# Kernel tuning notes

Measured on AMD Instinct MI355X. Metric: run time of the kernel, lower is better.

The kernel has to match this reference:

```python
import jax, jax.numpy as jnp
import numpy as np

N_NODES = 50000
N_EDGES = 600000
F_IN = 128
HID = 128
N_CLASSES = 10


def _gcn_graph(edge_index, n_nodes):
    # PyG GCNConv: add self-loops, deg computed on target (col) with weight 1,
    # norm_e = deg^-1/2[src] * deg^-1/2[dst]
    src = jnp.concatenate([edge_index[0], jnp.arange(n_nodes, dtype=edge_index.dtype)])
    dst = jnp.concatenate([edge_index[1], jnp.arange(n_nodes, dtype=edge_index.dtype)])
    deg = jax.ops.segment_sum(jnp.ones_like(dst, dtype=jnp.float32), dst, num_segments=n_nodes)
    dinv = jnp.where(deg > 0, jax.lax.rsqrt(deg), 0.0)
    norm = dinv[src] * dinv[dst]  # [E+N]
    return src, dst, norm


def _gcn_layer(x, W, b, src, dst, norm, n_nodes):
    h = x @ W                      # [N, out] linear first (bias applied post-agg)
    m = h[src] * norm[:, None]     # gather + scale, [E+N, out]
    out = jax.ops.segment_sum(m, dst, num_segments=n_nodes)  # scatter-add
    return out + b


def setup_inputs() -> dict:
    key = jax.random.key(0)
    ks = jax.random.split(key, 4)
    x = jax.random.normal(ks[0], (N_NODES, F_IN), dtype=jnp.float32)
    edge_index = jax.random.randint(ks[1], (2, N_EDGES), 0, N_NODES, dtype=jnp.int64)
    # Glorot-ish init scale for weights
    W_stack = jax.random.normal(ks[2], (8, HID, HID), dtype=jnp.float32) * (1.0 / np.sqrt(HID))
    b_stack = jnp.zeros((8, HID), dtype=jnp.float32)
    W_out = jax.random.normal(ks[3], (HID, N_CLASSES), dtype=jnp.float32) * (1.0 / np.sqrt(HID))
    b_out = jnp.zeros((N_CLASSES,), dtype=jnp.float32)
    return {"x": x, "edge_index": edge_index, "W_stack": W_stack, "b_stack": b_stack,
            "W_out": W_out, "b_out": b_out}


def reference(x, edge_index, W_stack, b_stack, W_out, b_out):
    n_nodes = x.shape[0]
    src, dst, norm = _gcn_graph(edge_index, n_nodes)
    h = x
    for i in range(8):  # conv1..conv8 with ELU
        h = jax.nn.elu(_gcn_layer(h, W_stack[i], b_stack[i], src, dst, norm, n_nodes))
    # conv9: no activation
    return _gcn_layer(h, W_out, b_out, src, dst, norm, n_nodes)
```

## Files before the change

### kernel.cpp

```cpp
#include <hip/hip_runtime.h>
#include <math.h>

#define NN 50000
#define NE 600000
#define HID 128
#define NCLS 10

typedef __bf16 bf16x8 __attribute__((ext_vector_type(8)));
typedef float f32x16 __attribute__((ext_vector_type(16)));

__device__ __forceinline__ void split3(float f, ushort& h, ushort& m, ushort& l) {
    unsigned uh = __float_as_uint(f) & 0xffff0000u;
    float fm = f - __uint_as_float(uh);
    unsigned um = __float_as_uint(fm) & 0xffff0000u;
    float fl = fm - __uint_as_float(um);
    h = (ushort)(uh >> 16);
    m = (ushort)(um >> 16);
    l = (ushort)(__float_as_uint(fl) >> 16);
}


__global__ __launch_bounds__(256) void k_count(const int* __restrict__ edge,
                                               int* __restrict__ counts) {
    int e = blockIdx.x * 256 + threadIdx.x;
    if (e < NE) atomicAdd(&counts[edge[NE + e]], 1);
}

__device__ __forceinline__ int wave_incl_scan(int x, int lane) {
#pragma unroll
    for (int off = 1; off < 64; off <<= 1) {
        int y = __shfl_up(x, off, 64);
        if (lane >= off) x += y;
    }
    return x;
}

__global__ __launch_bounds__(256) void k_scan1(const int* __restrict__ counts,
                                               int* __restrict__ rowptr,
                                               int* __restrict__ bsum,
                                               float* __restrict__ dinv) {
    __shared__ int ws[4];
    int tid = threadIdx.x;
    int i = blockIdx.x * 256 + tid;
    int lane = tid & 63, wv = tid >> 6;
    int v = (i < NN) ? counts[i] : 0;
    if (i < NN) dinv[i] = rsqrtf((float)(v + 1));
    int x = wave_incl_scan(v, lane);
    if (lane == 63) ws[wv] = x;
    __syncthreads();
    int off = 0;
    for (int j = 0; j < wv; ++j) off += ws[j];
    if (i < NN) rowptr[i] = off + x - v;
    if (tid == 255) bsum[blockIdx.x] = off + x;
}

__global__ __launch_bounds__(256) void k_scan2(int* __restrict__ bsum, int n) {
    __shared__ int ws[4];
    int tid = threadIdx.x;
    int lane = tid & 63, wv = tid >> 6;
    int v = (tid < n) ? bsum[tid] : 0;
    int x = wave_incl_scan(v, lane);
    if (lane == 63) ws[wv] = x;
    __syncthreads();
    int off = 0;
    for (int j = 0; j < wv; ++j) off += ws[j];
    __syncthreads();
    if (tid < n) bsum[tid] = off + x - v;
}

__global__ __launch_bounds__(256) void k_scan3(int* __restrict__ rowptr,
                                               const int* __restrict__ bsum) {
    int i = blockIdx.x * 256 + threadIdx.x;
    if (i < NN) rowptr[i] += bsum[blockIdx.x];
    if (i == 0) rowptr[NN] = NE;
}

__global__ __launch_bounds__(256) void k_fill(const int* __restrict__ edge,
                                              const int* __restrict__ rowptr,
                                              int* __restrict__ cursor,
                                              const float* __restrict__ dinv,
                                              int2* __restrict__ csr) {
    int e = blockIdx.x * 256 + threadIdx.x;
    if (e >= NE) return;
    int s = edge[e], d = edge[NE + e];
    int p = rowptr[d] + atomicAdd(&cursor[d], 1);
    csr[p] = make_int2(s, __float_as_int(dinv[s] * dinv[d]));
}


__global__ __launch_bounds__(256) void k_split_w(const float* __restrict__ Wst,
                                                 ushort* __restrict__ Wt3) {
    int i = blockIdx.x * 256 + threadIdx.x;
    if (i >= 8 * HID * HID) return;
    int l = i >> 14;
    int k = (i >> 7) & 127;
    int n = i & 127;
    ushort h, m, lo;
    split3(Wst[i], h, m, lo);
    size_t base = (size_t)l * 3 * HID * HID + (size_t)n * HID + k;
    Wt3[base] = h;
    Wt3[base + HID * HID] = m;
    Wt3[base + 2 * HID * HID] = lo;
}


__global__ __launch_bounds__(256) void k_mfma_gemm(const float* __restrict__ H,
                                                   const ushort* __restrict__ Wt,
                                                   float* __restrict__ T) {
    __shared__ ushort As[3][128][40];
    __shared__ ushort Bs[3][128][40];
    int tid = threadIdx.x;
    int lane = tid & 63, w = tid >> 6;
    int wy = w >> 1, wx = w & 1;
    int l31 = lane & 31, lh = lane >> 5;
    int rowbase = blockIdx.x * 128;

    int arow = tid >> 1;
    int kh = (tid & 1) * 16;
    int garow = rowbase + arow;
    if (garow >= NN) garow = NN - 1;
    size_t aoff = (size_t)garow * HID;

    f32x16 acc[2][2] = {};

    for (int k0 = 0; k0 < HID; k0 += 32) {
        const float4* asrc = (const float4*)(H + aoff + k0 + kh);
        float4 af0 = asrc[0], af1 = asrc[1], af2 = asrc[2], af3 = asrc[3];
        uint4 rb[6];
#pragma unroll
        for (int c = 0; c < 6; ++c) {
            int chunk = c * 256 + tid;
            int p = chunk >> 9;
            int rem = chunk & 511;
            int col = rem >> 2;
            int q = rem & 3;
            rb[c] = *(const uint4*)(Wt + p * (HID * HID) + col * HID + k0 + q * 8);
        }
        float av[16] = {af0.x, af0.y, af0.z, af0.w, af1.x, af1.y, af1.z, af1.w,
                        af2.x, af2.y, af2.z, af2.w, af3.x, af3.y, af3.z, af3.w};
        union { ushort u[16]; uint4 v[2]; } ph, pm, pl;
#pragma unroll
        for (int q = 0; q < 16; ++q) split3(av[q], ph.u[q], pm.u[q], pl.u[q]);

        __syncthreads();
        *(uint4*)&As[0][arow][kh] = ph.v[0];
        *(uint4*)&As[0][arow][kh + 8] = ph.v[1];
        *(uint4*)&As[1][arow][kh] = pm.v[0];
        *(uint4*)&As[1][arow][kh + 8] = pm.v[1];
        *(uint4*)&As[2][arow][kh] = pl.v[0];
        *(uint4*)&As[2][arow][kh + 8] = pl.v[1];
#pragma unroll
        for (int c = 0; c < 6; ++c) {
            int chunk = c * 256 + tid;
            int p = chunk >> 9;
            int rem = chunk & 511;
            int col = rem >> 2;
            int q = rem & 3;
            *(uint4*)&Bs[p][col][q * 8] = rb[c];
        }
        __syncthreads();

#pragma unroll
        for (int ks = 0; ks < 32; ks += 16) {
            int kk = ks + lh * 8;
            bf16x8 a[3][2], b[3][2];
#pragma unroll
            for (int p = 0; p < 3; ++p)
#pragma unroll
                for (int h = 0; h < 2; ++h) {
                    a[p][h] = *(const bf16x8*)&As[p][wy * 64 + h * 32 + l31][kk];
                    b[p][h] = *(const bf16x8*)&Bs[p][wx * 64 + h * 32 + l31][kk];
                }
#pragma unroll
            for (int h = 0; h < 2; ++h)
#pragma unroll
                for (int c = 0; c < 2; ++c)
                    acc[h][c] = __builtin_amdgcn_mfma_f32_32x32x16_bf16(a[0][h], b[0][c], acc[h][c], 0, 0, 0);
#pragma unroll
            for (int h = 0; h < 2; ++h)
#pragma unroll
                for (int c = 0; c < 2; ++c)
                    acc[h][c] = __builtin_amdgcn_mfma_f32_32x32x16_bf16(a[0][h], b[1][c], acc[h][c], 0, 0, 0);
#pragma unroll
            for (int h = 0; h < 2; ++h)
#pragma unroll
                for (int c = 0; c < 2; ++c)
                    acc[h][c] = __builtin_amdgcn_mfma_f32_32x32x16_bf16(a[1][h], b[0][c], acc[h][c], 0, 0, 0);
#pragma unroll
            for (int h = 0; h < 2; ++h)
#pragma unroll
                for (int c = 0; c < 2; ++c)
                    acc[h][c] = __builtin_amdgcn_mfma_f32_32x32x16_bf16(a[0][h], b[2][c], acc[h][c], 0, 0, 0);
#pragma unroll
            for (int h = 0; h < 2; ++h)
#pragma unroll
                for (int c = 0; c < 2; ++c)
                    acc[h][c] = __builtin_amdgcn_mfma_f32_32x32x16_bf16(a[1][h], b[1][c], acc[h][c], 0, 0, 0);
#pragma unroll
            for (int h = 0; h < 2; ++h)
#pragma unroll
                for (int c = 0; c < 2; ++c)
                    acc[h][c] = __builtin_amdgcn_mfma_f32_32x32x16_bf16(a[2][h], b[0][c], acc[h][c], 0, 0, 0);
        }
    }
#pragma unroll
    for (int h = 0; h < 2; ++h)
#pragma unroll
        for (int c = 0; c < 2; ++c)
#pragma unroll
            for (int reg = 0; reg < 16; ++reg) {
                int r = (reg & 3) + 8 * (reg >> 2) + 4 * lh;
                int gr = rowbase + wy * 64 + h * 32 + r;
                if (gr < NN)
                    T[(size_t)gr * HID + wx * 64 + c * 32 + l31] = acc[h][c][reg];
            }
}


__global__ __launch_bounds__(256) void k_gather_agg(const float* __restrict__ T,
                                                    float* __restrict__ Hout,
                                                    const int* __restrict__ rowptr,
                                                    const int2* __restrict__ csr,
                                                    const float* __restrict__ dinv,
                                                    const float* __restrict__ bias) {
    int node = (blockIdx.x * 256 + threadIdx.x) >> 5;
    if (node >= NN) return;
    int l31 = threadIdx.x & 31;

    int beg = rowptr[node], end = rowptr[node + 1];
    float sn = dinv[node];
    float4 bv = ((const float4*)bias)[l31];
    float4 tv = ((const float4*)(T + (size_t)node * HID))[l31];

    float4 acc = {0.f, 0.f, 0.f, 0.f};
    const int2 zed = make_int2(0, 0);

    int i = beg;
    int2 e0 = (i < end) ? csr[i] : zed;
    int2 e1 = (i + 1 < end) ? csr[i + 1] : zed;
    int2 e2 = (i + 2 < end) ? csr[i + 2] : zed;
    int2 e3 = (i + 3 < end) ? csr[i + 3] : zed;
    for (; i < end; i += 4) {
        float4 u0 = ((const float4*)(T + (size_t)e0.x * HID))[l31];
        float4 u1 = ((const float4*)(T + (size_t)e1.x * HID))[l31];
        float4 u2 = ((const float4*)(T + (size_t)e2.x * HID))[l31];
        float4 u3 = ((const float4*)(T + (size_t)e3.x * HID))[l31];
        float w0 = __int_as_float(e0.y), w1 = __int_as_float(e1.y);
        float w2 = __int_as_float(e2.y), w3 = __int_as_float(e3.y);
        e0 = (i + 4 < end) ? csr[i + 4] : zed;
        e1 = (i + 5 < end) ? csr[i + 5] : zed;
        e2 = (i + 6 < end) ? csr[i + 6] : zed;
        e3 = (i + 7 < end) ? csr[i + 7] : zed;
        acc.x += w0 * u0.x; acc.y += w0 * u0.y; acc.z += w0 * u0.z; acc.w += w0 * u0.w;
        acc.x += w1 * u1.x; acc.y += w1 * u1.y; acc.z += w1 * u1.z; acc.w += w1 * u1.w;
        acc.x += w2 * u2.x; acc.y += w2 * u2.y; acc.z += w2 * u2.z; acc.w += w2 * u2.w;
        acc.x += w3 * u3.x; acc.y += w3 * u3.y; acc.z += w3 * u3.z; acc.w += w3 * u3.w;
    }

    sn *= sn;
    float4 r;
    r.x = acc.x + sn * tv.x + bv.x;
    r.y = acc.y + sn * tv.y + bv.y;
    r.z = acc.z + sn * tv.z + bv.z;
    r.w = acc.w + sn * tv.w + bv.w;
    r.x = r.x > 0.f ? r.x : expm1f(r.x);
    r.y = r.y > 0.f ? r.y : expm1f(r.y);
    r.z = r.z > 0.f ? r.z : expm1f(r.z);
    r.w = r.w > 0.f ? r.w : expm1f(r.w);
    ((float4*)(Hout + (size_t)node * HID))[l31] = r;
}


__global__ __launch_bounds__(256) void k_matmul_out(const float* __restrict__ H,
                                                    const float* __restrict__ W,
                                                    float* __restrict__ T2) {
    __shared__ float Ws[128 * 11];
    int tid = threadIdx.x;
    for (int m = tid; m < HID * NCLS; m += 256) {
        int k = m / NCLS, c = m - k * NCLS;
        Ws[k * 11 + c] = W[m];
    }
    __syncthreads();
    int row = (blockIdx.x * 256 + tid) >> 4;
    int c16 = tid & 15;
    if (row >= NN) return;
    const float* h = H + (size_t)row * HID;
    float acc[NCLS];
#pragma unroll
    for (int c = 0; c < NCLS; ++c) acc[c] = 0.f;
#pragma unroll
    for (int j = 0; j < 8; ++j) {
        float hv = h[c16 + 16 * j];
        const float* wr = &Ws[(c16 + 16 * j) * 11];
#pragma unroll
        for (int c = 0; c < NCLS; ++c) acc[c] += hv * wr[c];
    }
#pragma unroll
    for (int off = 8; off >= 1; off >>= 1) {
#pragma unroll
        for (int c = 0; c < NCLS; ++c) acc[c] += __shfl_xor(acc[c], off, 16);
    }
    if (c16 < NCLS) T2[(size_t)row * NCLS + c16] = acc[c16];
}

__global__ __launch_bounds__(256) void k_gather_out(const float* __restrict__ T2,
                                                    float* __restrict__ out,
                                                    const int* __restrict__ rowptr,
                                                    const int2* __restrict__ csr,
                                                    const float* __restrict__ dinv,
                                                    const float* __restrict__ bias) {
    int lane = threadIdx.x & 63;
    int node = (blockIdx.x * 256 + threadIdx.x) >> 6;
    if (node >= NN) return;
    int slot = lane >> 4, c = lane & 15;
    int beg = rowptr[node], end = rowptr[node + 1];
    float acc = 0.f;
    if (c < NCLS) {
        for (int i = beg + slot; i < end; i += 4) {
            int2 e = csr[i];
            acc += __int_as_float(e.y) * T2[(size_t)e.x * NCLS + c];
        }
    }
    acc += __shfl_xor(acc, 16, 64);
    acc += __shfl_xor(acc, 32, 64);
    if (slot == 0 && c < NCLS) {
        float sn = dinv[node];
        sn *= sn;
        out[node * NCLS + c] = acc + sn * T2[(size_t)node * NCLS + c] + bias[c];
    }
}


extern "C" void kernel_launch(void* const* d_in, const int* in_sizes, int n_in,
                              void* d_out, int out_size, void* d_ws, size_t ws_size,
                              hipStream_t stream) {
    (void)in_sizes; (void)n_in; (void)out_size; (void)ws_size;
    const float* x       = (const float*)d_in[0];
    const int*   edge    = (const int*)d_in[1];
    const float* W_stack = (const float*)d_in[2];
    const float* b_stack = (const float*)d_in[3];
    const float* W_out   = (const float*)d_in[4];
    const float* b_out   = (const float*)d_in[5];
    float* out = (float*)d_out;

    char* ws = (char*)d_ws;
    const size_t bigbuf = (size_t)NN * HID * sizeof(float);
    float* X      = (float*)ws;
    float* Y      = (float*)(ws + bigbuf);
    char*  p      = ws + 2 * bigbuf;
    int2*  csr    = (int2*)p;              p += sizeof(int2) * NE;
    float* dinv   = (float*)p;             p += sizeof(float) * NN;
    int*   rowptr = (int*)p;               p += sizeof(int) * (NN + 1);
    int*   counts = (int*)p;               p += sizeof(int) * NN;
    int*   bsum   = (int*)p;               p += sizeof(int) * 256;
    p = (char*)(((size_t)p + 15) & ~(size_t)15);
    ushort* Wt3 = (ushort*)p;  p += sizeof(ushort) * 8 * 3 * HID * HID;

    const int NB_N  = (NN + 255) / 256;
    const int NB_E  = (NE + 255) / 256;
    const int NB_G  = (NN + 127) / 128;
    const int NB_A  = (NN * 32 + 255) / 256;
    const int NB_W  = (NN * 64 + 255) / 256;
    const int NB_O  = (NN * 16 + 255) / 256;
    const int NB_SW = (8 * HID * HID + 255) / 256;

    hipMemsetAsync(counts, 0, sizeof(int) * NN, stream);
    k_count<<<NB_E, 256, 0, stream>>>(edge, counts);
    k_scan1<<<NB_N, 256, 0, stream>>>(counts, rowptr, bsum, dinv);
    k_scan2<<<1, 256, 0, stream>>>(bsum, NB_N);
    k_scan3<<<NB_N, 256, 0, stream>>>(rowptr, bsum);
    hipMemsetAsync(counts, 0, sizeof(int) * NN, stream);
    k_fill<<<NB_E, 256, 0, stream>>>(edge, rowptr, counts, dinv, csr);

    k_split_w<<<NB_SW, 256, 0, stream>>>(W_stack, Wt3);

    const float* Hin = x;
    for (int l = 0; l < 8; ++l) {
        k_mfma_gemm<<<NB_G, 256, 0, stream>>>(Hin, Wt3 + (size_t)l * 3 * HID * HID, Y);
        k_gather_agg<<<NB_A, 256, 0, stream>>>(Y, X, rowptr, csr, dinv,
                                               b_stack + (size_t)l * HID);
        Hin = X;
    }

    k_matmul_out<<<NB_O, 256, 0, stream>>>(X, W_out, Y);
    k_gather_out<<<NB_W, 256, 0, stream>>>(Y, out, rowptr, csr, dinv, b_out);
}
```

Measured before the change: 788.8 us.

## Prefetch GEMM tiles, split aggregation across half-waves, drop cursor memset

The GEMM now loads the next k-slice of activations and split weights into registers while the current slice runs MFMAs, overlapping global loads with compute. The aggregation kernel uses a full 64-lane wave per node, with two half-waves each taking alternating edges and combining via a shuffle. This raises memory-level parallelism at the cost of twice as many threads. CSR fill counts down the existing degree counters with atomicSub, removing a memset. The output matmul reads contiguous float4 rows and pads T2 rows to 16 floats.

```diff
diff --git a/kernel.cpp b/kernel.cpp
--- a/kernel.cpp
+++ b/kernel.cpp
@@ -5,6 +5,7 @@
 #define NE 600000
 #define HID 128
 #define NCLS 10
+#define T2S 16
 
 typedef __bf16 bf16x8 __attribute__((ext_vector_type(8)));
 typedef float f32x16 __attribute__((ext_vector_type(16)));
@@ -83,8 +84,8 @@
     int e = blockIdx.x * 256 + threadIdx.x;
     if (e >= NE) return;
     int s = edge[e], d = edge[NE + e];
-    int p = rowptr[d] + atomicAdd(&cursor[d], 1);
-    csr[p] = make_int2(s, __float_as_int(dinv[s] * dinv[d]));
+    int slot = atomicSub(&cursor[d], 1) - 1;
+    csr[rowptr[d] + slot] = make_int2(s, __float_as_int(dinv[s] * dinv[d]));
 }
 
 
@@ -123,19 +124,23 @@
 
     f32x16 acc[2][2] = {};
 
+    float4 af0, af1, af2, af3;
+    {
+        const float4* asrc = (const float4*)(H + aoff + kh);
+        af0 = asrc[0]; af1 = asrc[1]; af2 = asrc[2]; af3 = asrc[3];
+    }
+    uint4 rb[6];
+#pragma unroll
+    for (int c = 0; c < 6; ++c) {
+        int chunk = c * 256 + tid;
+        int p = chunk >> 9;
+        int rem = chunk & 511;
+        int col = rem >> 2;
+        int q = rem & 3;
+        rb[c] = *(const uint4*)(Wt + p * (HID * HID) + col * HID + q * 8);
+    }
+
     for (int k0 = 0; k0 < HID; k0 += 32) {
-        const float4* asrc = (const float4*)(H + aoff + k0 + kh);
-        float4 af0 = asrc[0], af1 = asrc[1], af2 = asrc[2], af3 = asrc[3];
-        uint4 rb[6];
-#pragma unroll
-        for (int c = 0; c < 6; ++c) {
-            int chunk = c * 256 + tid;
-            int p = chunk >> 9;
-            int rem = chunk & 511;
-            int col = rem >> 2;
-            int q = rem & 3;
-            rb[c] = *(const uint4*)(Wt + p * (HID * HID) + col * HID + k0 + q * 8);
-        }
         float av[16] = {af0.x, af0.y, af0.z, af0.w, af1.x, af1.y, af1.z, af1.w,
                         af2.x, af2.y, af2.z, af2.w, af3.x, af3.y, af3.z, af3.w};
         union { ushort u[16]; uint4 v[2]; } ph, pm, pl;
@@ -160,6 +165,21 @@
         }
         __syncthreads();
 
+        int k0n = k0 + 32;
+        if (k0n < HID) {
+            const float4* asrc = (const float4*)(H + aoff + k0n + kh);
+            af0 = asrc[0]; af1 = asrc[1]; af2 = asrc[2]; af3 = asrc[3];
+#pragma unroll
+            for (int c = 0; c < 6; ++c) {
+                int chunk = c * 256 + tid;
+                int p = chunk >> 9;
+                int rem = chunk & 511;
+                int col = rem >> 2;
+                int q = rem & 3;
+                rb[c] = *(const uint4*)(Wt + p * (HID * HID) + col * HID + k0n + q * 8);
+            }
+        }
+
 #pragma unroll
         for (int ks = 0; ks < 32; ks += 16) {
             int kk = ks + lh * 8;
@@ -223,51 +243,61 @@
                                                     const int2* __restrict__ csr,
                                                     const float* __restrict__ dinv,
                                                     const float* __restrict__ bias) {
-    int node = (blockIdx.x * 256 + threadIdx.x) >> 5;
+    int lane = threadIdx.x & 63;
+    int node = (blockIdx.x * 256 + threadIdx.x) >> 6;
     if (node >= NN) return;
-    int l31 = threadIdx.x & 31;
+    int slot = lane >> 5, l31 = lane & 31;
 
     int beg = rowptr[node], end = rowptr[node + 1];
     float sn = dinv[node];
-    float4 bv = ((const float4*)bias)[l31];
-    float4 tv = ((const float4*)(T + (size_t)node * HID))[l31];
 
     float4 acc = {0.f, 0.f, 0.f, 0.f};
+    if (slot == 1) {
+        float4 tv = ((const float4*)(T + (size_t)node * HID))[l31];
+        float4 bv = ((const float4*)bias)[l31];
+        float s2 = sn * sn;
+        acc.x = s2 * tv.x + bv.x;
+        acc.y = s2 * tv.y + bv.y;
+        acc.z = s2 * tv.z + bv.z;
+        acc.w = s2 * tv.w + bv.w;
+    }
+
     const int2 zed = make_int2(0, 0);
-
-    int i = beg;
-    int2 e0 = (i < end) ? csr[i] : zed;
-    int2 e1 = (i + 1 < end) ? csr[i + 1] : zed;
-    int2 e2 = (i + 2 < end) ? csr[i + 2] : zed;
-    int2 e3 = (i + 3 < end) ? csr[i + 3] : zed;
-    for (; i < end; i += 4) {
+    int p = beg + slot;
+    int2 e0 = (p < end) ? csr[p] : zed;
+    int2 e1 = (p + 2 < end) ? csr[p + 2] : zed;
+    int2 e2 = (p + 4 < end) ? csr[p + 4] : zed;
+    int2 e3 = (p + 6 < end) ? csr[p + 6] : zed;
+    for (; p < end; p += 8) {
         float4 u0 = ((const float4*)(T + (size_t)e0.x * HID))[l31];
         float4 u1 = ((const float4*)(T + (size_t)e1.x * HID))[l31];
         float4 u2 = ((const float4*)(T + (size_t)e2.x * HID))[l31];
         float4 u3 = ((const float4*)(T + (size_t)e3.x * HID))[l31];
         float w0 = __int_as_float(e0.y), w1 = __int_as_float(e1.y);
         float w2 = __int_as_float(e2.y), w3 = __int_as_float(e3.y);
-        e0 = (i + 4 < end) ? csr[i + 4] : zed;
-        e1 = (i + 5 < end) ? csr[i + 5] : zed;
-        e2 = (i + 6 < end) ? csr[i + 6] : zed;
-        e3 = (i + 7 < end) ? csr[i + 7] : zed;
+        e0 = (p + 8 < end) ? csr[p + 8] : zed;
+        e1 = (p + 10 < end) ? csr[p + 10] : zed;
+        e2 = (p + 12 < end) ? csr[p + 12] : zed;
+        e3 = (p + 14 < end) ? csr[p + 14] : zed;
         acc.x += w0 * u0.x; acc.y += w0 * u0.y; acc.z += w0 * u0.z; acc.w += w0 * u0.w;
         acc.x += w1 * u1.x; acc.y += w1 * u1.y; acc.z += w1 * u1.z; acc.w += w1 * u1.w;
         acc.x += w2 * u2.x; acc.y += w2 * u2.y; acc.z += w2 * u2.z; acc.w += w2 * u2.w;
         acc.x += w3 * u3.x; acc.y += w3 * u3.y; acc.z += w3 * u3.z; acc.w += w3 * u3.w;
     }
 
-    sn *= sn;
-    float4 r;
-    r.x = acc.x + sn * tv.x + bv.x;
-    r.y = acc.y + sn * tv.y + bv.y;
-    r.z = acc.z + sn * tv.z + bv.z;
-    r.w = acc.w + sn * tv.w + bv.w;
-    r.x = r.x > 0.f ? r.x : expm1f(r.x);
-    r.y = r.y > 0.f ? r.y : expm1f(r.y);
-    r.z = r.z > 0.f ? r.z : expm1f(r.z);
-    r.w = r.w > 0.f ? r.w : expm1f(r.w);
-    ((float4*)(Hout + (size_t)node * HID))[l31] = r;
+    acc.x += __shfl_xor(acc.x, 32, 64);
+    acc.y += __shfl_xor(acc.y, 32, 64);
+    acc.z += __shfl_xor(acc.z, 32, 64);
+    acc.w += __shfl_xor(acc.w, 32, 64);
+
+    if (slot == 0) {
+        float4 r = acc;
+        r.x = r.x > 0.f ? r.x : expm1f(r.x);
+        r.y = r.y > 0.f ? r.y : expm1f(r.y);
+        r.z = r.z > 0.f ? r.z : expm1f(r.z);
+        r.w = r.w > 0.f ? r.w : expm1f(r.w);
+        ((float4*)(Hout + (size_t)node * HID))[l31] = r;
+    }
 }
 
 
@@ -284,23 +314,24 @@
     int row = (blockIdx.x * 256 + tid) >> 4;
     int c16 = tid & 15;
     if (row >= NN) return;
-    const float* h = H + (size_t)row * HID;
+    const float4* h4 = (const float4*)(H + (size_t)row * HID) + c16 * 2;
+    float4 h0 = h4[0], h1 = h4[1];
+    float hv[8] = {h0.x, h0.y, h0.z, h0.w, h1.x, h1.y, h1.z, h1.w};
     float acc[NCLS];
 #pragma unroll
     for (int c = 0; c < NCLS; ++c) acc[c] = 0.f;
 #pragma unroll
     for (int j = 0; j < 8; ++j) {
-        float hv = h[c16 + 16 * j];
-        const float* wr = &Ws[(c16 + 16 * j) * 11];
-#pragma unroll
-        for (int c = 0; c < NCLS; ++c) acc[c] += hv * wr[c];
+        const float* wr = &Ws[(c16 * 8 + j) * 11];
+#pragma unroll
+        for (int c = 0; c < NCLS; ++c) acc[c] += hv[j] * wr[c];
     }
 #pragma unroll
     for (int off = 8; off >= 1; off >>= 1) {
 #pragma unroll
         for (int c = 0; c < NCLS; ++c) acc[c] += __shfl_xor(acc[c], off, 16);
     }
-    if (c16 < NCLS) T2[(size_t)row * NCLS + c16] = acc[c16];
+    if (c16 < NCLS) T2[(size_t)row * T2S + c16] = acc[c16];
 }
 
 __global__ __launch_bounds__(256) void k_gather_out(const float* __restrict__ T2,
@@ -318,7 +349,7 @@
     if (c < NCLS) {
         for (int i = beg + slot; i < end; i += 4) {
             int2 e = csr[i];
-            acc += __int_as_float(e.y) * T2[(size_t)e.x * NCLS + c];
+            acc += __int_as_float(e.y) * T2[(size_t)e.x * T2S + c];
         }
     }
     acc += __shfl_xor(acc, 16, 64);
@@ -326,7 +357,7 @@
     if (slot == 0 && c < NCLS) {
         float sn = dinv[node];
         sn *= sn;
-        out[node * NCLS + c] = acc + sn * T2[(size_t)node * NCLS + c] + bias[c];
+        out[node * NCLS + c] = acc + sn * T2[(size_t)node * T2S + c] + bias[c];
     }
 }
 
@@ -359,7 +390,7 @@
     const int NB_N  = (NN + 255) / 256;
     const int NB_E  = (NE + 255) / 256;
     const int NB_G  = (NN + 127) / 128;
-    const int NB_A  = (NN * 32 + 255) / 256;
+    const int NB_A  = (NN * 64 + 255) / 256;
     const int NB_W  = (NN * 64 + 255) / 256;
     const int NB_O  = (NN * 16 + 255) / 256;
     const int NB_SW = (8 * HID * HID + 255) / 256;
@@ -369,7 +400,6 @@
     k_scan1<<<NB_N, 256, 0, stream>>>(counts, rowptr, bsum, dinv);
     k_scan2<<<1, 256, 0, stream>>>(bsum, NB_N);
     k_scan3<<<NB_N, 256, 0, stream>>>(rowptr, bsum);
-    hipMemsetAsync(counts, 0, sizeof(int) * NN, stream);
     k_fill<<<NB_E, 256, 0, stream>>>(edge, rowptr, counts, dinv, csr);
 
     k_split_w<<<NB_SW, 256, 0, stream>>>(W_stack, Wt3);
```

Result: no change. 800.1 us (+1.4%).
